# Performance work log

Measured on AMD Instinct MI355X. Metric: run time of the kernel, lower is better.

Reference implementation:

```python
import jax, jax.numpy as jnp
import numpy as np

B, T, C = 4, 2048, 1024
NH = 16
HD = C // NH  # 64


def setup_inputs() -> dict:
    key = jax.random.key(0)
    k1, k2, k3 = jax.random.split(key, 3)
    x = jax.random.normal(k1, (B, T, C), dtype=jnp.float32)
    # causal mask buffer, 1 = keep, 0 = mask out
    mask = jnp.tril(jnp.ones((T, T), dtype=jnp.int32))[None, None, :, :]
    # learned params (Linear with bias=False): torch stores weight as [out, in],
    # y = x @ W.T ; we store transposed for direct matmul
    w_qkv = jax.random.normal(k2, (C, 3 * C), dtype=jnp.float32) / np.sqrt(C)
    w_proj = jax.random.normal(k3, (C, C), dtype=jnp.float32) / np.sqrt(C)
    return {"x": x, "mask": mask, "w_qkv": w_qkv, "w_proj": w_proj}


def reference(x, mask, w_qkv, w_proj):
    b, t, c = x.shape
    qkv = x @ w_qkv  # [b, t, 3c]
    q, k, v = jnp.split(qkv, 3, axis=-1)
    # [b, nh, t, hd]
    q = q.reshape(b, t, NH, HD).transpose(0, 2, 1, 3)
    k = k.reshape(b, t, NH, HD).transpose(0, 2, 1, 3)
    v = v.reshape(b, t, NH, HD).transpose(0, 2, 1, 3)
    att = jnp.einsum("bhqd,bhkd->bhqk", q, k) * (1.0 / np.sqrt(HD))
    att = jnp.where(mask == 0, -jnp.inf, att)
    att = jax.nn.softmax(att, axis=-1)
    y = jnp.einsum("bhqk,bhkd->bhqd", att, v)
    y = y.transpose(0, 2, 1, 3).reshape(b, t, c)
    return y @ w_proj
```

## Files before the change

kernel.cpp:

```cpp
#include <hip/hip_runtime.h>
#include <hip/hip_bf16.h>

typedef _Float16 f16;
typedef __attribute__((ext_vector_type(4))) _Float16 f16x4;
typedef __attribute__((ext_vector_type(8))) _Float16 f16x8;
typedef __attribute__((ext_vector_type(4))) float f32x4;

#define MFMA16(a, b, c) __builtin_amdgcn_mfma_f32_16x16x16f16((a), (b), (c), 0, 0, 0)
#define MFMA32(a, b, c) __builtin_amdgcn_mfma_f32_16x16x32_f16((a), (b), (c), 0, 0, 0)
#define EXP2(x) __builtin_amdgcn_exp2f(x)
#define GLOAD_LDS16(g, l)                                                        \
  __builtin_amdgcn_global_load_lds((const __attribute__((address_space(1))) void*)(g), \
                                   (__attribute__((address_space(3))) void*)(l), 16, 0, 0)
typedef const __attribute__((address_space(3))) char* lds_cp;
#define TR16(dst, addr, imm) \
  asm volatile("ds_read_b64_tr_b16 %0, %1 offset:" imm : "=v"(dst) : "v"(addr))

__device__ __forceinline__ float max3f(float a, float b, float c) {
  return fmaxf(fmaxf(a, b), c);
}

__global__ __launch_bounds__(256) void prep_kernel(
    const float* __restrict__ x, f16* __restrict__ x16,
    const float* __restrict__ wq, f16* __restrict__ wqT,
    const float* __restrict__ wp, f16* __restrict__ wpT) {
  const int blk = blockIdx.x;
  const int tid = threadIdx.x;
  if (blk < 8192) {
    int i = blk * 256 + tid;
    const float4 v = reinterpret_cast<const float4*>(x)[i];
    f16x4 h;
    h[0] = (f16)v.x; h[1] = (f16)v.y; h[2] = (f16)v.z; h[3] = (f16)v.w;
    reinterpret_cast<f16x4*>(x16)[i] = h;
    return;
  }
  const float* src;
  f16* dst;
  int R, Cc, bx, by;
  if (blk < 11264) {
    int j = blk - 8192;
    bx = j % 96; by = j / 96;
    src = wq; dst = wqT; R = 1024; Cc = 3072;
  } else {
    int j = blk - 11264;
    bx = j & 31; by = j >> 5;
    src = wp; dst = wpT; R = 1024; Cc = 1024;
  }
  __shared__ float t[32][33];
  int tx0 = bx * 32, ty0 = by * 32;
  int c = tid & 31;
  int r0 = tid >> 5;
#pragma unroll
  for (int i = 0; i < 4; i++) {
    int r = r0 + 8 * i;
    t[r][c] = src[(size_t)(ty0 + r) * Cc + tx0 + c];
  }
  __syncthreads();
#pragma unroll
  for (int i = 0; i < 4; i++) {
    int a = r0 + 8 * i;
    dst[(size_t)(tx0 + a) * R + ty0 + c] = (f16)t[c][a];
  }
}

__global__ __launch_bounds__(512, 2) void gemm256_8ph_kernel(
    const f16* __restrict__ A, const f16* __restrict__ Bt, f16* __restrict__ C,
    int M, int N, int K) {
  __shared__ __align__(16) char smem[131072];
  const int tid = threadIdx.x;
  const int lane = tid & 63, wid = tid >> 6;
  const int wm = wid >> 2, wn = wid & 3;
  const int lo = lane & 15, hi = lane >> 4;

  const int ntn = N >> 8;
  const int nwg = (M >> 8) * ntn;
  const int wg = (blockIdx.x & 7) * (nwg >> 3) + (blockIdx.x >> 3);
  const int tm0 = (wg / ntn) << 8, tn0 = (wg % ntn) << 8;

  const int sr = tid >> 3;
  const int sc8 = (tid & 7) ^ (sr & 7);

  const int sw = lo & 7;
  const int aoff0 = wm * 16384 + lo * 128 + ((hi ^ sw) << 4);
  const int aoff1 = wm * 16384 + lo * 128 + (((4 + hi) ^ sw) << 4);
  const int brow = ((wn & 1) * 64 + lo) * 128;
  const int boff0 = 32768 + (wn >> 1) * 16384 + brow + ((hi ^ sw) << 4);
  const int boff1 = 32768 + (wn >> 1) * 16384 + brow + (((4 + hi) ^ sw) << 4);

  f32x4 acc[8][4] = {};

  const int nslots = K >> 4;
  auto stage_slot = [&](int s) {
    if (s >= nslots) return;
    const int kt = s >> 2, ct = s & 3;
    char* dst = smem + (kt & 1) * 65536 + ct * 16384 + tid * 16;
    const f16* src = (ct < 2) ? (A + (size_t)(tm0 + (ct & 1) * 128) * K)
                              : (Bt + (size_t)(tn0 + (ct & 1) * 128) * K);
    const f16* p = src + (size_t)sr * K + kt * 64 + sc8 * 8;
    GLOAD_LDS16(p, dst);
    GLOAD_LDS16(p + ((size_t)K << 6), dst + 8192);
  };

  auto ktile4 = [&](const char* db, int sb) {
    f16x8 a[4][2], bA[2][2], bB[2][2];
    asm volatile("s_waitcnt vmcnt(2)" ::: "memory");
    __builtin_amdgcn_s_barrier();
#pragma unroll
    for (int mi = 0; mi < 4; mi++) {
      a[mi][0] = *(const f16x8*)(db + aoff0 + mi * 2048);
      a[mi][1] = *(const f16x8*)(db + aoff1 + mi * 2048);
    }
#pragma unroll
    for (int nn = 0; nn < 2; nn++) {
      bA[nn][0] = *(const f16x8*)(db + boff0 + nn * 2048);
      bA[nn][1] = *(const f16x8*)(db + boff1 + nn * 2048);
    }
    stage_slot(sb);
    __builtin_amdgcn_s_barrier();
    asm volatile("s_waitcnt lgkmcnt(0)" ::: "memory");
    __builtin_amdgcn_sched_barrier(0);
    __builtin_amdgcn_s_setprio(1);
#pragma unroll
    for (int mi = 0; mi < 4; mi++)
#pragma unroll
      for (int nn = 0; nn < 2; nn++) {
        acc[mi][nn] = MFMA32(a[mi][0], bA[nn][0], acc[mi][nn]);
        acc[mi][nn] = MFMA32(a[mi][1], bA[nn][1], acc[mi][nn]);
      }
    __builtin_amdgcn_s_setprio(0);
    __builtin_amdgcn_s_barrier();
#pragma unroll
    for (int nn = 0; nn < 2; nn++) {
      bB[nn][0] = *(const f16x8*)(db + boff0 + (2 + nn) * 2048);
      bB[nn][1] = *(const f16x8*)(db + boff1 + (2 + nn) * 2048);
    }
    stage_slot(sb + 1);
    __builtin_amdgcn_s_barrier();
    asm volatile("s_waitcnt lgkmcnt(0)" ::: "memory");
    __builtin_amdgcn_sched_barrier(0);
    __builtin_amdgcn_s_setprio(1);
#pragma unroll
    for (int mi = 0; mi < 4; mi++)
#pragma unroll
      for (int nn = 0; nn < 2; nn++) {
        acc[mi][2 + nn] = MFMA32(a[mi][0], bB[nn][0], acc[mi][2 + nn]);
        acc[mi][2 + nn] = MFMA32(a[mi][1], bB[nn][1], acc[mi][2 + nn]);
      }
    __builtin_amdgcn_s_setprio(0);
    __builtin_amdgcn_s_barrier();
#pragma unroll
    for (int mi = 0; mi < 4; mi++) {
      a[mi][0] = *(const f16x8*)(db + aoff0 + 8192 + mi * 2048);
      a[mi][1] = *(const f16x8*)(db + aoff1 + 8192 + mi * 2048);
    }
    stage_slot(sb + 2);
    __builtin_amdgcn_s_barrier();
    asm volatile("s_waitcnt lgkmcnt(0)" ::: "memory");
    __builtin_amdgcn_sched_barrier(0);
    __builtin_amdgcn_s_setprio(1);
#pragma unroll
    for (int mi = 0; mi < 4; mi++)
#pragma unroll
      for (int nn = 0; nn < 2; nn++) {
        acc[4 + mi][nn] = MFMA32(a[mi][0], bA[nn][0], acc[4 + mi][nn]);
        acc[4 + mi][nn] = MFMA32(a[mi][1], bA[nn][1], acc[4 + mi][nn]);
      }
    __builtin_amdgcn_s_setprio(0);
    __builtin_amdgcn_s_barrier();
    stage_slot(sb + 3);
    __builtin_amdgcn_s_barrier();
    __builtin_amdgcn_s_setprio(1);
#pragma unroll
    for (int mi = 0; mi < 4; mi++)
#pragma unroll
      for (int nn = 0; nn < 2; nn++) {
        acc[4 + mi][2 + nn] = MFMA32(a[mi][0], bB[nn][0], acc[4 + mi][2 + nn]);
        acc[4 + mi][2 + nn] = MFMA32(a[mi][1], bB[nn][1], acc[4 + mi][2 + nn]);
      }
    __builtin_amdgcn_s_setprio(0);
  };

  for (int s = 0; s < 5; s++) stage_slot(s);
  asm volatile("s_waitcnt vmcnt(2)" ::: "memory");
  __builtin_amdgcn_s_barrier();

  const int NI = K >> 7;
  for (int t = 0; t < NI; t++) {
    ktile4(smem, 8 * t + 5);
    ktile4(smem + 65536, 8 * t + 9);
  }

#pragma unroll
  for (int mi = 0; mi < 8; mi++)
#pragma unroll
    for (int ni = 0; ni < 4; ni++)
#pragma unroll
      for (int r = 0; r < 4; r++) {
        int row = tm0 + wm * 128 + mi * 16 + 4 * hi + r;
        int col = tn0 + wn * 64 + ni * 16 + lo;
        C[(size_t)row * N + col] = (f16)acc[mi][ni][r];
      }
}

template <bool OUT_F32>
__global__ __launch_bounds__(256) void gemm_f16_kernel(
    const f16* __restrict__ A, const f16* __restrict__ Bt, void* __restrict__ Cout,
    int M, int N, int K) {
  constexpr int BK = 32;
  __shared__ f16 Al[3][128 * BK];
  __shared__ f16 Bl[3][128 * BK];

  const int tid = threadIdx.x;
  const int lane = tid & 63, wid = tid >> 6;
  const int wm = wid >> 1, wn = wid & 1;
  const int lo = lane & 15, hi = lane >> 4;
  const int tn0 = blockIdx.x * 128, tm0 = blockIdx.y * 128;

  f32x4 acc[4][4] = {};

  const int r1 = tid >> 2, o1 = (tid & 3) * 8;

  auto stage = [&](int kt, int c) {
    GLOAD_LDS16(&A[(size_t)(tm0 + r1) * K + kt + o1], &Al[c][tid * 8]);
    GLOAD_LDS16(&A[(size_t)(tm0 + r1 + 64) * K + kt + o1], &Al[c][(tid + 256) * 8]);
    GLOAD_LDS16(&Bt[(size_t)(tn0 + r1) * K + kt + o1], &Bl[c][tid * 8]);
    GLOAD_LDS16(&Bt[(size_t)(tn0 + r1 + 64) * K + kt + o1], &Bl[c][(tid + 256) * 8]);
  };

  auto compute = [&](int cur) {
    f16x8 af[4], bf[4];
#pragma unroll
    for (int mi = 0; mi < 4; mi++)
      af[mi] = *(const f16x8*)&Al[cur][(wm * 64 + mi * 16 + lo) * BK + 8 * hi];
#pragma unroll
    for (int ni = 0; ni < 4; ni++)
      bf[ni] = *(const f16x8*)&Bl[cur][(wn * 64 + ni * 16 + lo) * BK + 8 * hi];
    __builtin_amdgcn_s_setprio(1);
#pragma unroll
    for (int mi = 0; mi < 4; mi++)
#pragma unroll
      for (int ni = 0; ni < 4; ni++)
        acc[mi][ni] = MFMA32(af[mi], bf[ni], acc[mi][ni]);
    __builtin_amdgcn_s_setprio(0);
  };

  const int NT = K / BK;
  stage(0, 0);
  stage(BK, 1);

  int cur = 0;
  for (int t = 0; t < NT - 1; t++) {
    asm volatile("s_waitcnt vmcnt(4)" ::: "memory");
    __builtin_amdgcn_s_barrier();
    if (t + 2 < NT) stage((t + 2) * BK, (t + 2) % 3);
    compute(cur);
    cur = (cur == 2) ? 0 : cur + 1;
  }
  asm volatile("s_waitcnt vmcnt(0)" ::: "memory");
  __builtin_amdgcn_s_barrier();
  compute(cur);

#pragma unroll
  for (int mi = 0; mi < 4; mi++)
#pragma unroll
    for (int ni = 0; ni < 4; ni++)
#pragma unroll
      for (int r = 0; r < 4; r++) {
        int row = tm0 + wm * 64 + mi * 16 + 4 * hi + r;
        int col = tn0 + wn * 64 + ni * 16 + lo;
        float v = acc[mi][ni][r];
        if (OUT_F32)
          ((float*)Cout)[(size_t)row * N + col] = v;
        else
          ((f16*)Cout)[(size_t)row * N + col] = (f16)v;
      }
}

__global__ __launch_bounds__(256, 4) void attn_kernel(
    const f16* __restrict__ qkv, f16* __restrict__ y) {
  constexpr int T = 2048, NHD = 3072, LDO = 72;
  const int bh = blockIdx.x;
  const int b = bh >> 4, h = bh & 15;
  const int pr = blockIdx.y;
  const int tid = threadIdx.x;
  const int lane = tid & 63, w = tid >> 6;
  const int lo = lane & 15, hi = lane >> 4;

  const size_t base = (size_t)b * T * NHD + (size_t)h * 64;
  const f16* Qp = qkv + base;
  const f16* Kp = qkv + base + 1024;
  const f16* Vp = qkv + base + 2048;

  __shared__ __align__(16) char smem[32768];
  f16 (*Ol)[LDO] = (f16(*)[LDO])smem;

  const int tile[2] = {pr, 31 - pr};
  const int qb[2] = {tile[0] * 64 + w * 16, tile[1] * 64 + w * 16};

  const float scf = 0.125f * 1.44269504089f;
  f16x8 qf[2][2];
#pragma unroll
  for (int s = 0; s < 2; s++) {
    const f16* qrow = Qp + (size_t)(qb[s] + lo) * NHD;
#pragma unroll
    for (int ks = 0; ks < 2; ks++) {
      f16x8 v = *(const f16x8*)&qrow[ks * 32 + 8 * hi];
#pragma unroll
      for (int j = 0; j < 8; j++) v[j] = (f16)((float)v[j] * scf);
      qf[s][ks] = v;
    }
  }

  f32x4 oacc[2][4] = {};
  f32x4 lacc[2] = {};
  float mreg[2] = {-1e30f, -1e30f};
  const f16x4 ones4 = {(f16)1.f, (f16)1.f, (f16)1.f, (f16)1.f};

  const int kr = tid >> 3;
  const int kslot = (tid & 7) ^ (kr & 7);
  const int tp = tid & 127;
  const int vkey = 4 * (tp >> 3) + ((tp >> 1) & 3);
  const int vcol = (tid >> 7) * 16 + (tid & 1) * 8;

  const int kfo0 = lo * 64 + ((hi ^ (lo & 7)) * 8);
  const int kfo1 = lo * 64 + (((4 + hi) ^ (lo & 7)) * 8);

  auto stage = [&](int kv, int c) {
    char* kb = smem + c * 8192;
    char* vb = smem + 16384 + c * 8192;
    GLOAD_LDS16(&Kp[(size_t)(kv + kr) * NHD + kslot * 8], kb + tid * 16);
    GLOAD_LDS16(&Kp[(size_t)(kv + kr + 32) * NHD + kslot * 8], kb + 4096 + tid * 16);
    GLOAD_LDS16(&Vp[(size_t)(kv + vkey) * NHD + vcol], vb + tid * 16);
    GLOAD_LDS16(&Vp[(size_t)(kv + vkey) * NHD + vcol + 32], vb + 4096 + tid * 16);
  };

  const int nt = 32 - pr;
  stage(0, 0);
  asm volatile("s_waitcnt vmcnt(0)" ::: "memory");
  __builtin_amdgcn_s_barrier();

  for (int t = 0; t < nt; t++) {
    const int cur = t & 1;
    const int kv0 = t * 64;
    if (t + 1 < nt) stage(kv0 + 64, cur ^ 1);

    const f16* Kl = (const f16*)(smem + cur * 8192);
    const bool act0 = kv0 <= qb[0] + 15;

    f16x8 kf[2][4];
#pragma unroll
    for (int ct = 0; ct < 4; ct++) {
      kf[0][ct] = *(const f16x8*)&Kl[ct * 1024 + kfo0];
      kf[1][ct] = *(const f16x8*)&Kl[ct * 1024 + kfo1];
    }

    f16x4 pb[2][4];
#pragma unroll
    for (int s = 0; s < 2; s++) {
      if (s == 0 && !act0) continue;
      f32x4 s_[4] = {};
      __builtin_amdgcn_s_setprio(1);
#pragma unroll
      for (int ks = 0; ks < 2; ks++)
#pragma unroll
        for (int ct = 0; ct < 4; ct++)
          s_[ct] = MFMA32(kf[ks][ct], qf[s][ks], s_[ct]);
      __builtin_amdgcn_s_setprio(0);

      if (kv0 + 63 > qb[s]) {
        const int q = qb[s] + lo;
#pragma unroll
        for (int ct = 0; ct < 4; ct++)
#pragma unroll
          for (int r = 0; r < 4; r++)
            if (kv0 + ct * 16 + 4 * hi + r > q) s_[ct][r] = -3.0e38f;
      }
      float t0 = max3f(s_[0][0], s_[0][1], s_[0][2]);
      float t1 = max3f(s_[0][3], s_[1][0], s_[1][1]);
      float t2 = max3f(s_[1][2], s_[1][3], s_[2][0]);
      float t3 = max3f(s_[2][1], s_[2][2], s_[2][3]);
      float t4 = max3f(s_[3][0], s_[3][1], s_[3][2]);
      float mt = fmaxf(max3f(t0, t1, t2), max3f(t3, t4, s_[3][3]));
      mt = fmaxf(mt, __shfl_xor(mt, 16));
      mt = fmaxf(mt, __shfl_xor(mt, 32));
      float mn = mreg[s];
      if (!__all(mt <= mn + 8.f)) {
        mn = fmaxf(mn, mt);
        const float al = EXP2(mreg[s] - mn);
        mreg[s] = mn;
#pragma unroll
        for (int r = 0; r < 4; r++) lacc[s][r] *= al;
#pragma unroll
        for (int ct = 0; ct < 4; ct++)
#pragma unroll
          for (int r = 0; r < 4; r++) oacc[s][ct][r] *= al;
      }
#pragma unroll
      for (int ct = 0; ct < 4; ct++)
#pragma unroll
        for (int r = 0; r < 4; r++)
          pb[s][ct][r] = (f16)EXP2(s_[ct][r] - mn);
      __builtin_amdgcn_s_setprio(1);
#pragma unroll
      for (int kk = 0; kk < 4; kk++)
        lacc[s] = MFMA16(ones4, pb[s][kk], lacc[s]);
      __builtin_amdgcn_s_setprio(0);
    }

    lds_cp vtrb = (lds_cp)(smem + 16384 + cur * 8192) + lane * 8;
#pragma unroll
    for (int ct = 0; ct < 4; ct++) {
      lds_cp bct = vtrb + ct * 2048;
      f16x4 v0, v1, v2, v3;
      TR16(v0, bct, "0");
      TR16(v1, bct, "512");
      TR16(v2, bct, "1024");
      TR16(v3, bct, "1536");
      asm volatile("s_waitcnt lgkmcnt(0)" ::: "memory");
      __builtin_amdgcn_sched_barrier(0);
      __builtin_amdgcn_s_setprio(1);
      if (act0) {
        oacc[0][ct] = MFMA16(v0, pb[0][0], oacc[0][ct]);
        oacc[0][ct] = MFMA16(v1, pb[0][1], oacc[0][ct]);
        oacc[0][ct] = MFMA16(v2, pb[0][2], oacc[0][ct]);
        oacc[0][ct] = MFMA16(v3, pb[0][3], oacc[0][ct]);
      }
      oacc[1][ct] = MFMA16(v0, pb[1][0], oacc[1][ct]);
      oacc[1][ct] = MFMA16(v1, pb[1][1], oacc[1][ct]);
      oacc[1][ct] = MFMA16(v2, pb[1][2], oacc[1][ct]);
      oacc[1][ct] = MFMA16(v3, pb[1][3], oacc[1][ct]);
      __builtin_amdgcn_s_setprio(0);
    }

    asm volatile("s_waitcnt vmcnt(0)" ::: "memory");
    __builtin_amdgcn_s_barrier();
  }

#pragma unroll
  for (int s = 0; s < 2; s++) {
    __syncthreads();
    const float inv = 1.f / lacc[s][0];
#pragma unroll
    for (int ct = 0; ct < 4; ct++) {
      f16x4 o4;
#pragma unroll
      for (int r = 0; r < 4; r++) o4[r] = (f16)(oacc[s][ct][r] * inv);
      *(f16x4*)&Ol[w * 16 + lo][ct * 16 + 4 * hi] = o4;
    }
    __syncthreads();
#pragma unroll
    for (int i = 0; i < 2; i++) {
      int idx = tid + 256 * i;
      int qq = idx >> 3, ch = idx & 7;
      *(f16x8*)&y[((size_t)b * T + tile[s] * 64 + qq) * 1024 + (size_t)h * 64 + ch * 8] =
          *(const f16x8*)&Ol[qq][ch * 8];
    }
  }
}

extern "C" void kernel_launch(void* const* d_in, const int* in_sizes, int n_in,
                              void* d_out, int out_size, void* d_ws, size_t ws_size,
                              hipStream_t stream) {
  const float* x = (const float*)d_in[0];
  const float* w_qkv = (const float*)d_in[2];
  const float* w_proj = (const float*)d_in[3];

  constexpr int B = 4, T = 2048, C = 1024, NH = 16;
  constexpr int M = B * T;
  constexpr int N1 = 3 * C;

  char* ws = (char*)d_ws;
  f16* x16 = (f16*)ws;    ws += (size_t)M * C * 2;
  f16* wqkvT = (f16*)ws;  ws += (size_t)N1 * C * 2;
  f16* wprojT = (f16*)ws; ws += (size_t)C * C * 2;
  f16* qkvb = (f16*)ws;   ws += (size_t)M * N1 * 2;
  f16* y16 = (f16*)ws;

  prep_kernel<<<12288, 256, 0, stream>>>(x, x16, w_qkv, wqkvT, w_proj, wprojT);
  gemm256_8ph_kernel<<<(M / 256) * (N1 / 256), 512, 0, stream>>>(x16, wqkvT, qkvb, M, N1, C);
  attn_kernel<<<dim3(B * NH, 16), 256, 0, stream>>>(qkvb, y16);
  gemm_f16_kernel<true><<<dim3(C / 128, M / 128), 256, 0, stream>>>(y16, wprojT, (float*)d_out, M, C, C);
}
```

Measured before the change: 171.5 us.

## Retile QKV GEMM to 256x192 with simpler double-buffered pipeline

Changes the QKV projection GEMM tile from 256x256 to 256x192, so the launch has 512 workgroups instead of 384 to reduce wave quantization across CUs. The multi-slot staged load schedule is replaced by a two-buffer loop that loads the next A and B tiles during the two MFMA phases of each k-step. LDS use drops, but the loop waits for all outstanding global loads each iteration, which may expose more memory latency, and the smaller N tile lowers arithmetic intensity.

```diff
diff --git a/kernel.cpp b/kernel.cpp
--- a/kernel.cpp
+++ b/kernel.cpp
@@ -63,141 +63,119 @@
   }
 }
 
-__global__ __launch_bounds__(512, 2) void gemm256_8ph_kernel(
+__global__ __launch_bounds__(512, 2) void gemm_qkv_kernel(
     const f16* __restrict__ A, const f16* __restrict__ Bt, f16* __restrict__ C,
     int M, int N, int K) {
-  __shared__ __align__(16) char smem[131072];
+  __shared__ __align__(16) char smem[114688];
   const int tid = threadIdx.x;
   const int lane = tid & 63, wid = tid >> 6;
   const int wm = wid >> 2, wn = wid & 3;
   const int lo = lane & 15, hi = lane >> 4;
 
-  const int ntn = N >> 8;
+  const int ntn = N / 192;
   const int nwg = (M >> 8) * ntn;
   const int wg = (blockIdx.x & 7) * (nwg >> 3) + (blockIdx.x >> 3);
-  const int tm0 = (wg / ntn) << 8, tn0 = (wg % ntn) << 8;
-
-  const int sr = tid >> 3;
-  const int sc8 = (tid & 7) ^ (sr & 7);
-
-  const int sw = lo & 7;
-  const int aoff0 = wm * 16384 + lo * 128 + ((hi ^ sw) << 4);
-  const int aoff1 = wm * 16384 + lo * 128 + (((4 + hi) ^ sw) << 4);
-  const int brow = ((wn & 1) * 64 + lo) * 128;
-  const int boff0 = 32768 + (wn >> 1) * 16384 + brow + ((hi ^ sw) << 4);
-  const int boff1 = 32768 + (wn >> 1) * 16384 + brow + (((4 + hi) ^ sw) << 4);
-
-  f32x4 acc[8][4] = {};
-
-  const int nslots = K >> 4;
-  auto stage_slot = [&](int s) {
-    if (s >= nslots) return;
-    const int kt = s >> 2, ct = s & 3;
-    char* dst = smem + (kt & 1) * 65536 + ct * 16384 + tid * 16;
-    const f16* src = (ct < 2) ? (A + (size_t)(tm0 + (ct & 1) * 128) * K)
-                              : (Bt + (size_t)(tn0 + (ct & 1) * 128) * K);
-    const f16* p = src + (size_t)sr * K + kt * 64 + sc8 * 8;
-    GLOAD_LDS16(p, dst);
-    GLOAD_LDS16(p + ((size_t)K << 6), dst + 8192);
+  const int tm0 = (wg / ntn) << 8;
+  const int tn0 = (wg % ntn) * 192;
+
+  const int prow = tid >> 3;
+  const int u8 = (tid & 7) ^ (prow & 7);
+  const f16* asrc[4];
+  const f16* bsrc[3];
+#pragma unroll
+  for (int c = 0; c < 4; c++) asrc[c] = A + (size_t)(tm0 + c * 64 + prow) * K + u8 * 8;
+#pragma unroll
+  for (int c = 0; c < 3; c++) bsrc[c] = Bt + (size_t)(tn0 + c * 64 + prow) * K + u8 * 8;
+
+  const int swz = lo & 7;
+  const int s0 = (hi ^ swz) << 4, s1 = ((4 + hi) ^ swz) << 4;
+  const int aoff0 = wm * 16384 + lo * 128 + s0;
+  const int aoff1 = wm * 16384 + lo * 128 + s1;
+  int boff0[3], boff1[3];
+#pragma unroll
+  for (int ni = 0; ni < 3; ni++) {
+    int cr = 3 * wn + ni;
+    int base = 32768 + (cr >> 2) * 8192 + ((cr & 3) * 16 + lo) * 128;
+    boff0[ni] = base + s0;
+    boff1[ni] = base + s1;
+  }
+
+  f32x4 acc[8][3] = {};
+
+  auto stageA = [&](int kt, char* buf) {
+#pragma unroll
+    for (int c = 0; c < 4; c++)
+      GLOAD_LDS16(asrc[c] + kt, buf + c * 8192 + tid * 16);
   };
-
-  auto ktile4 = [&](const char* db, int sb) {
-    f16x8 a[4][2], bA[2][2], bB[2][2];
-    asm volatile("s_waitcnt vmcnt(2)" ::: "memory");
+  auto stageB = [&](int kt, char* buf) {
+#pragma unroll
+    for (int c = 0; c < 3; c++)
+      GLOAD_LDS16(bsrc[c] + kt, buf + 32768 + c * 8192 + tid * 16);
+  };
+
+  const int NT = K >> 6;
+  stageA(0, smem);
+  stageB(0, smem);
+
+  for (int t = 0; t < NT; t++) {
+    char* db = smem + (t & 1) * 57344;
+    char* nb = smem + ((t + 1) & 1) * 57344;
+    const int kt1 = (t + 1) << 6;
+
+    asm volatile("s_waitcnt vmcnt(0)" ::: "memory");
     __builtin_amdgcn_s_barrier();
+    f16x8 a[4][2], b[3][2];
 #pragma unroll
     for (int mi = 0; mi < 4; mi++) {
       a[mi][0] = *(const f16x8*)(db + aoff0 + mi * 2048);
       a[mi][1] = *(const f16x8*)(db + aoff1 + mi * 2048);
     }
 #pragma unroll
-    for (int nn = 0; nn < 2; nn++) {
-      bA[nn][0] = *(const f16x8*)(db + boff0 + nn * 2048);
-      bA[nn][1] = *(const f16x8*)(db + boff1 + nn * 2048);
-    }
-    stage_slot(sb);
-    __builtin_amdgcn_s_barrier();
+    for (int ni = 0; ni < 3; ni++) {
+      b[ni][0] = *(const f16x8*)(db + boff0[ni]);
+      b[ni][1] = *(const f16x8*)(db + boff1[ni]);
+    }
+    if (t + 1 < NT) stageA(kt1, nb);
     asm volatile("s_waitcnt lgkmcnt(0)" ::: "memory");
     __builtin_amdgcn_sched_barrier(0);
     __builtin_amdgcn_s_setprio(1);
 #pragma unroll
     for (int mi = 0; mi < 4; mi++)
 #pragma unroll
-      for (int nn = 0; nn < 2; nn++) {
-        acc[mi][nn] = MFMA32(a[mi][0], bA[nn][0], acc[mi][nn]);
-        acc[mi][nn] = MFMA32(a[mi][1], bA[nn][1], acc[mi][nn]);
+      for (int ni = 0; ni < 3; ni++) {
+        acc[mi][ni] = MFMA32(a[mi][0], b[ni][0], acc[mi][ni]);
+        acc[mi][ni] = MFMA32(a[mi][1], b[ni][1], acc[mi][ni]);
       }
     __builtin_amdgcn_s_setprio(0);
+
     __builtin_amdgcn_s_barrier();
 #pragma unroll
-    for (int nn = 0; nn < 2; nn++) {
-      bB[nn][0] = *(const f16x8*)(db + boff0 + (2 + nn) * 2048);
-      bB[nn][1] = *(const f16x8*)(db + boff1 + (2 + nn) * 2048);
-    }
-    stage_slot(sb + 1);
-    __builtin_amdgcn_s_barrier();
+    for (int mi = 0; mi < 4; mi++) {
+      a[mi][0] = *(const f16x8*)(db + aoff0 + 8192 + mi * 2048);
+      a[mi][1] = *(const f16x8*)(db + aoff1 + 8192 + mi * 2048);
+    }
+    if (t + 1 < NT) stageB(kt1, nb);
     asm volatile("s_waitcnt lgkmcnt(0)" ::: "memory");
     __builtin_amdgcn_sched_barrier(0);
     __builtin_amdgcn_s_setprio(1);
 #pragma unroll
     for (int mi = 0; mi < 4; mi++)
 #pragma unroll
-      for (int nn = 0; nn < 2; nn++) {
-        acc[mi][2 + nn] = MFMA32(a[mi][0], bB[nn][0], acc[mi][2 + nn]);
-        acc[mi][2 + nn] = MFMA32(a[mi][1], bB[nn][1], acc[mi][2 + nn]);
+      for (int ni = 0; ni < 3; ni++) {
+        acc[4 + mi][ni] = MFMA32(a[mi][0], b[ni][0], acc[4 + mi][ni]);
+        acc[4 + mi][ni] = MFMA32(a[mi][1], b[ni][1], acc[4 + mi][ni]);
       }
     __builtin_amdgcn_s_setprio(0);
-    __builtin_amdgcn_s_barrier();
-#pragma unroll
-    for (int mi = 0; mi < 4; mi++) {
-      a[mi][0] = *(const f16x8*)(db + aoff0 + 8192 + mi * 2048);
-      a[mi][1] = *(const f16x8*)(db + aoff1 + 8192 + mi * 2048);
-    }
-    stage_slot(sb + 2);
-    __builtin_amdgcn_s_barrier();
-    asm volatile("s_waitcnt lgkmcnt(0)" ::: "memory");
-    __builtin_amdgcn_sched_barrier(0);
-    __builtin_amdgcn_s_setprio(1);
-#pragma unroll
-    for (int mi = 0; mi < 4; mi++)
-#pragma unroll
-      for (int nn = 0; nn < 2; nn++) {
-        acc[4 + mi][nn] = MFMA32(a[mi][0], bA[nn][0], acc[4 + mi][nn]);
-        acc[4 + mi][nn] = MFMA32(a[mi][1], bA[nn][1], acc[4 + mi][nn]);
-      }
-    __builtin_amdgcn_s_setprio(0);
-    __builtin_amdgcn_s_barrier();
-    stage_slot(sb + 3);
-    __builtin_amdgcn_s_barrier();
-    __builtin_amdgcn_s_setprio(1);
-#pragma unroll
-    for (int mi = 0; mi < 4; mi++)
-#pragma unroll
-      for (int nn = 0; nn < 2; nn++) {
-        acc[4 + mi][2 + nn] = MFMA32(a[mi][0], bB[nn][0], acc[4 + mi][2 + nn]);
-        acc[4 + mi][2 + nn] = MFMA32(a[mi][1], bB[nn][1], acc[4 + mi][2 + nn]);
-      }
-    __builtin_amdgcn_s_setprio(0);
-  };
-
-  for (int s = 0; s < 5; s++) stage_slot(s);
-  asm volatile("s_waitcnt vmcnt(2)" ::: "memory");
-  __builtin_amdgcn_s_barrier();
-
-  const int NI = K >> 7;
-  for (int t = 0; t < NI; t++) {
-    ktile4(smem, 8 * t + 5);
-    ktile4(smem + 65536, 8 * t + 9);
   }
 
 #pragma unroll
   for (int mi = 0; mi < 8; mi++)
 #pragma unroll
-    for (int ni = 0; ni < 4; ni++)
+    for (int ni = 0; ni < 3; ni++)
 #pragma unroll
       for (int r = 0; r < 4; r++) {
         int row = tm0 + wm * 128 + mi * 16 + 4 * hi + r;
-        int col = tn0 + wn * 64 + ni * 16 + lo;
+        int col = tn0 + wn * 48 + ni * 16 + lo;
         C[(size_t)row * N + col] = (f16)acc[mi][ni][r];
       }
 }
@@ -477,7 +455,7 @@
   f16* y16 = (f16*)ws;
 
   prep_kernel<<<12288, 256, 0, stream>>>(x, x16, w_qkv, wqkvT, w_proj, wprojT);
-  gemm256_8ph_kernel<<<(M / 256) * (N1 / 256), 512, 0, stream>>>(x16, wqkvT, qkvb, M, N1, C);
+  gemm_qkv_kernel<<<(M / 256) * (N1 / 192), 512, 0, stream>>>(x16, wqkvT, qkvb, M, N1, C);
   attn_kernel<<<dim3(B * NH, 16), 256, 0, stream>>>(qkvb, y16);
   gemm_f16_kernel<true><<<dim3(C / 128, M / 128), 256, 0, stream>>>(y16, wprojT, (float*)d_out, M, C, C);
 }
```

Result: no change. 173.2 us (+1.0%).
